# Performance work log

Measured on AMD Instinct MI355X. Metric: run time of the kernel, lower is better.

## Reference

```python
import jax, jax.numpy as jnp
import numpy as np
import math

B, S, H, DK, NB = 2, 128, 4, 128, 4
D = H * DK  # 512


def setup_inputs() -> dict:
    key = jax.random.key(0)
    ks = jax.random.split(key, 24)
    g = lambda i, sh, std=1.0: jax.random.normal(ks[i], sh, jnp.float32) * std
    u = lambda i, sh: jax.random.uniform(ks[i], sh, jnp.float32)
    return {
        "x_m": g(0, (B, S, D)), "x_c": g(1, (B, S, D)),
        "b_m": g(2, (B, S, D)), "b_c": g(3, (B, S, D)),
        "bb_m": g(4, (B, NB, NB, D)), "bb_c": u(5, (B, NB, NB, D)),
        "p_m": g(6, (B, S, D)), "p_c": u(7, (B, S, D)),
        "W_xm": g(8, (3, D, H, DK), 0.02), "W_xc": g(9, (3, D, H, DK), 0.02),
        "W_bm": g(10, (3, D, H, DK), 0.02), "W_bc": g(11, (3, D, H, DK), 0.02),
        "Wq1_w": g(12, (DK, DK), 0.05), "Wq1_b": g(13, (DK,), 0.02),
        "Wq2_w": g(14, (DK, DK), 0.05), "Wq2_b": g(15, (DK,), 0.02),
        "Wk1_w": g(16, (DK, DK), 0.05), "Wk1_b": g(17, (DK,), 0.02),
        "Wk2_w": g(18, (DK, DK), 0.05), "Wk2_b": g(19, (DK,), 0.02),
        "mean_w": g(20, (D, D), 0.02), "mean_b": jnp.zeros((D,), jnp.float32),
        "cov_w": g(21, (D, D), 0.02), "cov_b": jnp.zeros((D,), jnp.float32),
        "ln_w": jnp.ones((D,), jnp.float32), "ln_b": jnp.zeros((D,), jnp.float32),
        "b_seq": jax.random.randint(ks[22], (B, S), 0, NB),
    }


def _elu1(x):
    return jax.nn.elu(x) + 1.0


def _tri_sagp(m1, m2, m3, c1, c2, c3):
    # fuse three diagonal Gaussians by product-of-Gaussians (precision-weighted)
    eps = 1e-24
    p1 = 1.0 / jnp.clip(c1, eps)
    p2 = 1.0 / jnp.clip(c2, eps)
    p3 = 1.0 / jnp.clip(c3, eps)
    c = 1.0 / (p1 + p2 + p3)
    return c * (m1 * p1 + m2 * p2 + m3 * p3), c


def _ln(x, w, b):
    m = jnp.mean(x, -1, keepdims=True)
    v = jnp.mean((x - m) ** 2, -1, keepdims=True)
    return (x - m) / jnp.sqrt(v + 1e-12) * w + b


def _forward(x_m, x_c, b_m, b_c, bb_m, bb_c, p_m, p_c,
             W_xm, W_xc, W_bm, W_bc,
             Wq1_w, Wq1_b, Wq2_w, Wq2_b, Wk1_w, Wk1_b, Wk2_w, Wk2_b,
             mean_w, mean_b, cov_w, cov_b, ln_w, ln_b, b_seq):
    Bb, Ss, Dd = x_m.shape
    Hh, Dk = W_xm.shape[2], W_xm.shape[3]
    proj = lambda x, w: jnp.einsum('bnd,dhk->bhnk', x, w)
    q1 = proj(x_m, W_xm[0]) + proj(b_m, W_bm[0])
    k1 = proj(x_m, W_xm[1]) + proj(b_m, W_bm[1])
    v1 = proj(x_m, W_xm[2]) + proj(b_m, W_bm[2])
    q2 = _elu1(proj(x_c, W_xc[0]) + proj(b_c, W_bc[0]))
    k2 = _elu1(proj(x_c, W_xc[1]) + proj(b_c, W_bc[1]))
    v2 = _elu1(proj(x_c, W_xc[2]) + proj(b_c, W_bc[2]))
    nb = bb_m.shape[1]
    # [B,NB,NB,D] -> [B,H,NB,NB,DK]
    bbm = bb_m.reshape(Bb, nb, nb, Hh, Dk).transpose(0, 3, 1, 2, 4)
    bbc = bb_c.reshape(Bb, nb, nb, Hh, Dk).transpose(0, 3, 1, 2, 4)
    # out[b,h,i,j,:] = bbm[b,h,b_seq[b,j],b_seq[b,i],:]  (matches torch advanced indexing + permute)
    gather = jax.vmap(lambda bb, seq: bb[:, seq[None, :], seq[:, None], :])
    bbm_b = gather(bbm, b_seq)  # [B,H,S,S,DK]
    bbc_b = gather(bbc, b_seq)
    pm = p_m.reshape(Bb, Ss, Hh, Dk).transpose(0, 2, 1, 3)  # [B,H,S,DK]
    pc = p_c.reshape(Bb, Ss, Hh, Dk).transpose(0, 2, 1, 3)
    lin = lambda x, w, b: x @ w.T + b
    fQm, fQc = _tri_sagp(q1[:, :, :, None, :], lin(bbm_b, Wq1_w, Wq1_b),
                         lin(pm, Wq2_w, Wq2_b)[:, :, :, None, :],
                         q2[:, :, :, None, :], bbc_b, pc[:, :, :, None, :])
    fKm, fKc = _tri_sagp(k1[:, :, None, :, :], lin(bbm_b, Wk1_w, Wk1_b),
                         lin(pm, Wk2_w, Wk2_b)[:, :, None, :, :],
                         k2[:, :, None, :, :], bbc_b, pc[:, :, None, :, :])
    eps = 1e-24
    # 2-Wasserstein^2 between diagonal Gaussians (the 1x1 matmul form reduces to this)
    w2 = jnp.sum((fQm - fKm) ** 2, -1) + jnp.sum(
        (jnp.sqrt(jnp.clip(fQc, eps)) - jnp.sqrt(jnp.clip(fKc, eps))) ** 2, -1)
    scores = -w2 / math.sqrt(Dk)  # [B,H,S,S]
    probs = jax.nn.softmax(scores, axis=-1)
    mean_ctx = jnp.einsum('bhij,bhjk->bhik', probs, v1)
    cov_ctx = jnp.einsum('bhij,bhjk->bhik', probs ** 2, v2)
    mean_ctx = mean_ctx.transpose(0, 2, 1, 3).reshape(Bb, Ss, Dd)
    cov_ctx = cov_ctx.transpose(0, 2, 1, 3).reshape(Bb, Ss, Dd)
    mean_h = _ln(mean_ctx @ mean_w.T + mean_b + x_m, ln_w, ln_b)
    cov_h = _ln(cov_ctx @ cov_w.T + cov_b + x_c, ln_w, ln_b)
    return mean_h, cov_h, probs


def reference(x_m, x_c, b_m, b_c, bb_m, bb_c, p_m, p_c,
              W_xm, W_xc, W_bm, W_bc,
              Wq1_w, Wq1_b, Wq2_w, Wq2_b, Wk1_w, Wk1_b, Wk2_w, Wk2_b,
              mean_w, mean_b, cov_w, cov_b, ln_w, ln_b, b_seq):
    return _forward(x_m, x_c, b_m, b_c, bb_m, bb_c, p_m, p_c,
                    W_xm, W_xc, W_bm, W_bc,
                    Wq1_w, Wq1_b, Wq2_w, Wq2_b, Wk1_w, Wk1_b, Wk2_w, Wk2_b,
                    mean_w, mean_b, cov_w, cov_b, ln_w, ln_b, b_seq)
```

## Files before the change

### kernel.cpp

```cpp
#include <hip/hip_runtime.h>
#include <math.h>

#define B_ 2
#define S_ 128
#define H_ 4
#define DK_ 128
#define NB_ 4
#define D_ 512
#define M_ 256

typedef __attribute__((ext_vector_type(8))) short short8;
typedef __attribute__((ext_vector_type(4))) float float4v;
typedef __attribute__((ext_vector_type(4))) unsigned short ushort4v;

__device__ __forceinline__ float elu1(float x) {
    return (x > 0.f) ? (x + 1.f) : __expf(x);
}

__device__ __forceinline__ unsigned short f2bf(float f) {
    unsigned u = __float_as_uint(f);
    unsigned r = (u + 0x7FFFu + ((u >> 16) & 1u)) >> 16;
    return (unsigned short)r;
}


__global__ __launch_bounds__(256) void k_prep(
    const float* __restrict__ x_m, const float* __restrict__ b_m,
    const float* __restrict__ x_c, const float* __restrict__ b_c,
    const float* __restrict__ mean_w, const float* __restrict__ cov_w,
    const float* __restrict__ W_xm, const float* __restrict__ W_xc,
    const float* __restrict__ W_bm, const float* __restrict__ W_bc,
    const float* __restrict__ p_m, const float* __restrict__ bb_m,
    const float* __restrict__ Wq2, const float* __restrict__ Wk2,
    const float* __restrict__ Wq1, const float* __restrict__ Wk1,
    unsigned short* __restrict__ A_m, unsigned short* __restrict__ A_c,
    unsigned short* __restrict__ wm_bf, unsigned short* __restrict__ wc_bf,
    unsigned short* __restrict__ Wt,
    unsigned short* __restrict__ pm_bf, unsigned short* __restrict__ bbm_bf,
    unsigned short* __restrict__ w4_bf)
{
    __shared__ unsigned short tile4[4][32][33];
    const int t = threadIdx.x;
    const int blk = blockIdx.x;
    const int NBK = gridDim.x;

    for (int cid = blk * 256 + t; cid < 315392; cid += NBK * 256) {
        const float* srcp;
        unsigned short* dstp;
        if (cid < 262144) {
            int job = cid >> 16;
            int off = (cid & 65535) * 4;
            if (job <= 1) {
                int m = off >> 10, k = off & 1023;
                if (job == 0) { srcp = (k < 512) ? (x_m + m * 512 + k) : (b_m + m * 512 + k - 512); dstp = A_m + off; }
                else          { srcp = (k < 512) ? (x_c + m * 512 + k) : (b_c + m * 512 + k - 512); dstp = A_c + off; }
            } else if (job == 2) { srcp = mean_w + off; dstp = wm_bf + off; }
            else                 { srcp = cov_w + off;  dstp = wc_bf + off; }
        } else if (cid < 294912) {
            int off = (cid - 262144) * 4;
            srcp = p_m + off; dstp = pm_bf + off;
        } else if (cid < 299008) {
            int off = (cid - 294912) * 4;
            srcp = bb_m + off; dstp = bbm_bf + off;
        } else {
            int off = (cid - 299008) * 4;
            int seg = off >> 14;
            const float* Ws = (seg == 0) ? Wq2 : (seg == 1) ? Wk2 : (seg == 2) ? Wq1 : Wk1;
            srcp = Ws + (off & 16383); dstp = w4_bf + off;
        }
        float4 v = *(const float4*)srcp;
        ushort4v o4;
        o4.x = f2bf(v.x); o4.y = f2bf(v.y); o4.z = f2bf(v.z); o4.w = f2bf(v.w);
        *(ushort4v*)dstp = o4;
    }

    const int tx = t & 31, ty = t >> 5;
#pragma unroll
    for (int it = 0; it < 4; ++it) {
        int tid = blk + it * 768;
        int nt = tid & 15, kt = (tid >> 4) & 15, z = tid >> 8;
        int o = z >> 1, part = z & 1;
        const float* src;
        if (part == 0) src = (o < 3) ? (W_xm + o * 262144) : (W_xc + (o - 3) * 262144);
        else           src = (o < 3) ? (W_bm + o * 262144) : (W_bc + (o - 3) * 262144);
#pragma unroll
        for (int u = 0; u < 4; ++u)
            tile4[it][ty + u * 8][tx] = f2bf(src[(kt * 32 + ty + u * 8) * 512 + nt * 32 + tx]);
    }
    __syncthreads();
#pragma unroll
    for (int it = 0; it < 4; ++it) {
        int tid = blk + it * 768;
        int nt = tid & 15, kt = (tid >> 4) & 15, z = tid >> 8;
        int o = z >> 1, part = z & 1;
        unsigned short* dst = Wt + o * 524288 + part * 512;
#pragma unroll
        for (int u = 0; u < 4; ++u)
            dst[(nt * 32 + ty + u * 8) * 1024 + kt * 32 + tx] = tile4[it][tx][ty + u * 8];
    }
}

__global__ __launch_bounds__(256) void k_mm(
    const unsigned short* __restrict__ A_m, const unsigned short* __restrict__ A_c,
    const unsigned short* __restrict__ Wt,
    const unsigned short* __restrict__ pm_bf, const unsigned short* __restrict__ bbm_bf,
    const unsigned short* __restrict__ w4_bf,
    const float* __restrict__ bq2, const float* __restrict__ bk2,
    const float* __restrict__ bq1, const float* __restrict__ bk1,
    float* __restrict__ qkv, float* __restrict__ pq, float* __restrict__ pk,
    float* __restrict__ bbq, float* __restrict__ bbk)
{
    const int t = threadIdx.x;
    const int wid = blockIdx.x * 4 + (t >> 6);
    const int lane = t & 63;
    const int l15 = lane & 15, quad = lane >> 4;

    if (wid < 3072) {
        const int o = wid >> 9;
        const int rem = wid & 511;
        const int nt = rem & 31, mt = rem >> 5;
        const int m0 = mt * 16, n0 = nt * 16;

        const unsigned short* A = (o < 3) ? A_m : A_c;
        const unsigned short* ap = A + (m0 + l15) * 1024 + quad * 8;
        const unsigned short* bp = Wt + o * 524288 + (n0 + l15) * 1024 + quad * 8;

        float4v acc0 = {0.f, 0.f, 0.f, 0.f};
        float4v acc1 = {0.f, 0.f, 0.f, 0.f};
#pragma unroll
        for (int k0 = 0; k0 < 1024; k0 += 64) {
            short8 a0 = *(const short8*)(ap + k0);
            short8 b0 = *(const short8*)(bp + k0);
            short8 a1 = *(const short8*)(ap + k0 + 32);
            short8 b1 = *(const short8*)(bp + k0 + 32);
            acc0 = __builtin_amdgcn_mfma_f32_16x16x32_bf16(a0, b0, acc0, 0, 0, 0);
            acc1 = __builtin_amdgcn_mfma_f32_16x16x32_bf16(a1, b1, acc1, 0, 0, 0);
        }
        float* dst = qkv + o * 131072;
#pragma unroll
        for (int r = 0; r < 4; ++r) {
            float v = acc0[r] + acc1[r];
            if (o >= 3) v = elu1(v);
            dst[(m0 + quad * 4 + r) * 512 + n0 + l15] = v;
        }
    } else {
        const unsigned short* Abf;
        const unsigned short* Wb;
        const float* bias;
        float* dst;
        int m0, n0, h;
        if (wid < 4096) {
            int lid = wid - 3072;
            int sel = lid >> 9;
            int r = lid & 511;
            h = r >> 7;
            int rem = r & 127;
            m0 = (rem >> 3) * 16; n0 = (rem & 7) * 16;
            Abf = pm_bf;
            Wb = w4_bf + sel * 16384;
            bias = sel ? bk2 : bq2;
            dst = sel ? pk : pq;
        } else {
            int lid = wid - 4096;
            int sel = lid >> 6;
            int r = lid & 63;
            h = r >> 4;
            int rem = r & 15;
            m0 = (rem >> 3) * 16; n0 = (rem & 7) * 16;
            Abf = bbm_bf;
            Wb = w4_bf + 32768 + sel * 16384;
            bias = sel ? bk1 : bq1;
            dst = sel ? bbk : bbq;
        }
        const unsigned short* ap = Abf + (m0 + l15) * 512 + h * 128 + quad * 8;
        const unsigned short* bp = Wb + (n0 + l15) * 128 + quad * 8;

        float4v acc0 = {0.f, 0.f, 0.f, 0.f};
        float4v acc1 = {0.f, 0.f, 0.f, 0.f};
#pragma unroll
        for (int k0 = 0; k0 < 128; k0 += 64) {
            short8 a0 = *(const short8*)(ap + k0);
            short8 b0 = *(const short8*)(bp + k0);
            short8 a1 = *(const short8*)(ap + k0 + 32);
            short8 b1 = *(const short8*)(bp + k0 + 32);
            acc0 = __builtin_amdgcn_mfma_f32_16x16x32_bf16(a0, b0, acc0, 0, 0, 0);
            acc1 = __builtin_amdgcn_mfma_f32_16x16x32_bf16(a1, b1, acc1, 0, 0, 0);
        }
        float bv = bias[n0 + l15];
#pragma unroll
        for (int r = 0; r < 4; ++r)
            dst[(m0 + quad * 4 + r) * 512 + h * 128 + n0 + l15] = acc0[r] + acc1[r] + bv;
    }
}

__global__ __launch_bounds__(128) void k_fuseK(
    const float* __restrict__ qkv, const float* __restrict__ pk,
    const float* __restrict__ bbk, const float* __restrict__ bb_c,
    const float* __restrict__ p_c, const int* __restrict__ b_seq,
    float* __restrict__ fKm, float* __restrict__ fKs)
{
    const int t = threadIdx.x;
    const int j = blockIdx.x, h = blockIdx.y, b = blockIdx.z;
    const int d = h * 128 + t;
    const float eps = 1e-24f;
    const int base = (b * S_ + j) * D_ + d;
    const int sj = b_seq[b * S_ + j];

    float m1 = qkv[M_ * D_ + base];
    float c1 = qkv[4 * M_ * D_ + base];
    float m3 = pk[base];
    float c3 = p_c[base];

    float p1 = 1.f / fmaxf(c1, eps);
    float p3 = 1.f / fmaxf(c3, eps);
    float mp13 = m1 * p1 + m3 * p3;

#pragma unroll
    for (int sv = 0; sv < 4; ++sv) {
        int idx = (b * 16 + sj * 4 + sv) * 512 + d;
        float m2 = bbk[idx];
        float c2 = bb_c[idx];
        float p2 = 1.f / fmaxf(c2, eps);
        float cc = 1.f / (p1 + p2 + p3);
        int o = (((b * H_ + h) * 4 + sv) * S_ + j) * 128 + t;
        fKm[o] = cc * (mp13 + m2 * p2);
        fKs[o] = sqrtf(fmaxf(cc, eps));
    }
}

__global__ __launch_bounds__(128) void k_attn3(
    const float* __restrict__ qkv, const float* __restrict__ pq,
    const float* __restrict__ bbq, const float* __restrict__ bb_c,
    const float* __restrict__ p_c, const int* __restrict__ b_seq,
    const float* __restrict__ fKm, const float* __restrict__ fKs,
    float* __restrict__ probs_out, unsigned short* __restrict__ mctxb,
    unsigned short* __restrict__ cctxb)
{
    const int t = threadIdx.x;
    const int i = blockIdx.x, h = blockIdx.y, b = blockIdx.z;
    const float eps = 1e-24f;

    __shared__ __attribute__((aligned(16))) float qm[4 * 132];
    __shared__ __attribute__((aligned(16))) float qs[4 * 132];
    __shared__ float red[4];
    __shared__ float pr[128], pr2[128];

    const int si = b_seq[b * S_ + i];
    const int sj = b_seq[b * S_ + t];

    {
        const int d = h * 128 + t;
        const int base = (b * S_ + i) * D_ + d;
        float m1 = qkv[base];
        float c1 = qkv[3 * M_ * D_ + base];
        float m3 = pq[base];
        float c3 = p_c[base];
        float p1 = 1.f / fmaxf(c1, eps);
        float p3 = 1.f / fmaxf(c3, eps);
        float mp13 = m1 * p1 + m3 * p3;
#pragma unroll
        for (int sv = 0; sv < 4; ++sv) {
            int idx = (b * 16 + sv * 4 + si) * 512 + d;
            float m2 = bbq[idx];
            float c2 = bb_c[idx];
            float p2 = 1.f / fmaxf(c2, eps);
            float cc = 1.f / (p1 + p2 + p3);
            qm[sv * 132 + t] = cc * (mp13 + m2 * p2);
            qs[sv * 132 + t] = sqrtf(fmaxf(cc, eps));
        }
    }
    __syncthreads();

    const int krow = (((b * H_ + h) * 4 + si) * S_ + t) * 128;
    const float4* kmp = (const float4*)(fKm + krow);
    const float4* ksp = (const float4*)(fKs + krow);

    float w2 = 0.f;
#pragma unroll 4
    for (int k4 = 0; k4 < 32; ++k4) {
        float4 km = kmp[k4];
        float4 ks = ksp[k4];
        float4 m = *(const float4*)&qm[sj * 132 + k4 * 4];
        float4 s = *(const float4*)&qs[sj * 132 + k4 * 4];
        float d0 = m.x - km.x, d1 = m.y - km.y, d2 = m.z - km.z, d3 = m.w - km.w;
        float e0 = s.x - ks.x, e1 = s.y - ks.y, e2 = s.z - ks.z, e3 = s.w - ks.w;
        w2 += d0 * d0 + d1 * d1 + d2 * d2 + d3 * d3
            + e0 * e0 + e1 * e1 + e2 * e2 + e3 * e3;
    }
    float score = -w2 * 0.08838834764831845f;

    float mx = score;
#pragma unroll
    for (int off = 32; off >= 1; off >>= 1) mx = fmaxf(mx, __shfl_xor(mx, off));
    if ((t & 63) == 0) red[t >> 6] = mx;
    __syncthreads();
    mx = fmaxf(red[0], red[1]);
    float e = __expf(score - mx);
    float sm = e;
#pragma unroll
    for (int off = 32; off >= 1; off >>= 1) sm += __shfl_xor(sm, off);
    if ((t & 63) == 0) red[2 + (t >> 6)] = sm;
    __syncthreads();
    float p = e / (red[2] + red[3]);

    probs_out[((b * H_ + h) * S_ + i) * S_ + t] = p;
    pr[t] = p;
    pr2[t] = p * p;
    __syncthreads();

    const float* v1 = qkv + 2 * M_ * D_ + (b * S_) * D_ + h * 128 + t;
    const float* v2 = qkv + 5 * M_ * D_ + (b * S_) * D_ + h * 128 + t;
    float am = 0.f, ac = 0.f;
#pragma unroll 8
    for (int j = 0; j < 128; ++j) {
        am = fmaf(pr[j], v1[j * D_], am);
        ac = fmaf(pr2[j], v2[j * D_], ac);
    }
    mctxb[(b * S_ + i) * D_ + h * 128 + t] = f2bf(am);
    cctxb[(b * S_ + i) * D_ + h * 128 + t] = f2bf(ac);
}

__global__ __launch_bounds__(256) void k_fin_mm(
    const unsigned short* __restrict__ mctxb, const unsigned short* __restrict__ cctxb,
    const unsigned short* __restrict__ wm_bf, const unsigned short* __restrict__ wc_bf,
    float* __restrict__ y_m, float* __restrict__ y_c)
{
    const int t = threadIdx.x;
    const int wid = blockIdx.x * 4 + (t >> 6);
    const int lane = t & 63;
    const int mat = wid >> 9;
    const int rem = wid & 511;
    const int nt = rem & 31, mt = rem >> 5;
    const int m0 = mt * 16, n0 = nt * 16;
    const int l15 = lane & 15, quad = lane >> 4;

    const unsigned short* A = mat ? cctxb : mctxb;
    const unsigned short* Bw = mat ? wc_bf : wm_bf;
    float* y = mat ? y_c : y_m;

    const unsigned short* ap = A + (m0 + l15) * 512 + quad * 8;
    const unsigned short* bp = Bw + (n0 + l15) * 512 + quad * 8;

    float4v acc0 = {0.f, 0.f, 0.f, 0.f};
    float4v acc1 = {0.f, 0.f, 0.f, 0.f};
#pragma unroll
    for (int k0 = 0; k0 < 512; k0 += 64) {
        short8 a0 = *(const short8*)(ap + k0);
        short8 b0 = *(const short8*)(bp + k0);
        short8 a1 = *(const short8*)(ap + k0 + 32);
        short8 b1 = *(const short8*)(bp + k0 + 32);
        acc0 = __builtin_amdgcn_mfma_f32_16x16x32_bf16(a0, b0, acc0, 0, 0, 0);
        acc1 = __builtin_amdgcn_mfma_f32_16x16x32_bf16(a1, b1, acc1, 0, 0, 0);
    }
#pragma unroll
    for (int r = 0; r < 4; ++r)
        y[(m0 + quad * 4 + r) * 512 + n0 + l15] = acc0[r] + acc1[r];
}

__global__ __launch_bounds__(256) void k_ln(
    const float* __restrict__ y_m, const float* __restrict__ y_c,
    const float* __restrict__ mean_b, const float* __restrict__ cov_b,
    const float* __restrict__ x_m, const float* __restrict__ x_c,
    const float* __restrict__ ln_w, const float* __restrict__ ln_b,
    float* __restrict__ out)
{
    const int t = threadIdx.x;
    const int id = blockIdx.x;
    const int mat = id >> 8, row = id & 255;
    const float* yg = mat ? y_c : y_m;
    const float* bias = mat ? cov_b : mean_b;
    const float* res = mat ? x_c : x_m;
    const int base = row * 512;

    __shared__ float red[8];

    float y0 = yg[base + t] + bias[t] + res[base + t];
    float y1 = yg[base + 256 + t] + bias[256 + t] + res[base + 256 + t];
    float s = y0 + y1, ss = y0 * y0 + y1 * y1;
#pragma unroll
    for (int off = 32; off >= 1; off >>= 1) { s += __shfl_xor(s, off); ss += __shfl_xor(ss, off); }
    if ((t & 63) == 0) { red[t >> 6] = s; red[4 + (t >> 6)] = ss; }
    __syncthreads();
    float mu = (red[0] + red[1] + red[2] + red[3]) * (1.f / 512.f);
    float var = (red[4] + red[5] + red[6] + red[7]) * (1.f / 512.f) - mu * mu;
    float rstd = 1.f / sqrtf(var + 1e-12f);
    out[mat * 131072 + base + t] = (y0 - mu) * rstd * ln_w[t] + ln_b[t];
    out[mat * 131072 + base + 256 + t] = (y1 - mu) * rstd * ln_w[256 + t] + ln_b[256 + t];
}

extern "C" void kernel_launch(void* const* d_in, const int* in_sizes, int n_in,
                              void* d_out, int out_size, void* d_ws, size_t ws_size,
                              hipStream_t stream) {
    (void)in_sizes; (void)n_in; (void)out_size; (void)ws_size;
    const float* x_m   = (const float*)d_in[0];
    const float* x_c   = (const float*)d_in[1];
    const float* b_m   = (const float*)d_in[2];
    const float* b_c   = (const float*)d_in[3];
    const float* bb_m  = (const float*)d_in[4];
    const float* bb_c  = (const float*)d_in[5];
    const float* p_m   = (const float*)d_in[6];
    const float* p_c   = (const float*)d_in[7];
    const float* W_xm  = (const float*)d_in[8];
    const float* W_xc  = (const float*)d_in[9];
    const float* W_bm  = (const float*)d_in[10];
    const float* W_bc  = (const float*)d_in[11];
    const float* Wq1_w = (const float*)d_in[12];
    const float* Wq1_b = (const float*)d_in[13];
    const float* Wq2_w = (const float*)d_in[14];
    const float* Wq2_b = (const float*)d_in[15];
    const float* Wk1_w = (const float*)d_in[16];
    const float* Wk1_b = (const float*)d_in[17];
    const float* Wk2_w = (const float*)d_in[18];
    const float* Wk2_b = (const float*)d_in[19];
    const float* mean_w = (const float*)d_in[20];
    const float* mean_b = (const float*)d_in[21];
    const float* cov_w  = (const float*)d_in[22];
    const float* cov_b  = (const float*)d_in[23];
    const float* ln_w   = (const float*)d_in[24];
    const float* ln_b   = (const float*)d_in[25];
    const int*   b_seq  = (const int*)d_in[26];

    float* ws = (float*)d_ws;
    float* qkv = ws;
    float* pq  = ws + 786432;
    float* pk  = ws + 917504;
    float* bbq = ws + 1048576;
    float* bbk = ws + 1064960;
    float* fKm = ws + 1081344;
    float* fKs = ws + 1605632;
    float* y_m = ws + 2129920;
    float* y_c = ws + 2260992;
    unsigned short* A_m    = (unsigned short*)(ws + 2392064);
    unsigned short* A_c    = (unsigned short*)(ws + 2523136);
    unsigned short* Wt     = (unsigned short*)(ws + 2654208);
    unsigned short* wm_bf  = (unsigned short*)(ws + 4227072);
    unsigned short* wc_bf  = (unsigned short*)(ws + 4358144);
    unsigned short* mctxb  = (unsigned short*)(ws + 4489216);
    unsigned short* cctxb  = (unsigned short*)(ws + 4554752);
    unsigned short* pm_bf  = (unsigned short*)(ws + 4620288);
    unsigned short* bbm_bf = (unsigned short*)(ws + 4685824);
    unsigned short* w4_bf  = (unsigned short*)(ws + 4694016);
    float* out = (float*)d_out;

    k_prep<<<dim3(768), 256, 0, stream>>>(
        x_m, b_m, x_c, b_c, mean_w, cov_w, W_xm, W_xc, W_bm, W_bc,
        p_m, bb_m, Wq2_w, Wk2_w, Wq1_w, Wk1_w,
        A_m, A_c, wm_bf, wc_bf, Wt, pm_bf, bbm_bf, w4_bf);
    k_mm<<<dim3(1056), 256, 0, stream>>>(
        A_m, A_c, Wt, pm_bf, bbm_bf, w4_bf,
        Wq2_b, Wk2_b, Wq1_b, Wk1_b,
        qkv, pq, pk, bbq, bbk);
    k_fuseK<<<dim3(128, 4, 2), 128, 0, stream>>>(
        qkv, pk, bbk, bb_c, p_c, b_seq, fKm, fKs);
    k_attn3<<<dim3(128, 4, 2), 128, 0, stream>>>(
        qkv, pq, bbq, bb_c, p_c, b_seq, fKm, fKs, out + 262144, mctxb, cctxb);
    k_fin_mm<<<dim3(256), 256, 0, stream>>>(
        mctxb, cctxb, wm_bf, wc_bf, y_m, y_c);
    k_ln<<<dim3(512), 256, 0, stream>>>(
        y_m, y_c, mean_b, cov_b, x_m, x_c, ln_w, ln_b, out);
}
```

Measured before the change: 176.0 us.

## Widen QKV GEMM wave tiles to 16x32, swizzle blocks for XCD locality

Each wave in the main projection GEMM now computes a 16x32 output tile, reusing the A fragment across two B column tiles, which halves the wave count and the redundant A loads. The first 384 blocks are remapped with a stride permutation so that blocks landing on the same XCD share A/W rows in cache. The attention kernel moves from a 3D grid to a 1D grid with batch and head interleaved in the low bits, also aimed at cache locality across XCDs. The cost is more accumulator registers per wave and fewer waves to hide memory latency.

After: 176.2 us, median of 2. No clear change (+0.1%).

```diff
diff --git a/kernel.cpp b/kernel.cpp
--- a/kernel.cpp
+++ b/kernel.cpp
@@ -111,37 +111,48 @@
     float* __restrict__ bbq, float* __restrict__ bbk)
 {
     const int t = threadIdx.x;
-    const int wid = blockIdx.x * 4 + (t >> 6);
+    const int blk = blockIdx.x;
+    const int sblk = (blk < 384) ? ((blk & 7) * 48 + (blk >> 3)) : blk;
+    const int wid = sblk * 4 + (t >> 6);
     const int lane = t & 63;
     const int l15 = lane & 15, quad = lane >> 4;
 
-    if (wid < 3072) {
-        const int o = wid >> 9;
-        const int rem = wid & 511;
-        const int nt = rem & 31, mt = rem >> 5;
-        const int m0 = mt * 16, n0 = nt * 16;
+    if (wid < 1536) {
+        const int o = wid >> 8;
+        const int rem = wid & 255;
+        const int nt2 = rem & 15, mt = rem >> 4;
+        const int m0 = mt * 16, n0 = nt2 * 32;
 
         const unsigned short* A = (o < 3) ? A_m : A_c;
-        const unsigned short* ap = A + (m0 + l15) * 1024 + quad * 8;
-        const unsigned short* bp = Wt + o * 524288 + (n0 + l15) * 1024 + quad * 8;
-
-        float4v acc0 = {0.f, 0.f, 0.f, 0.f};
-        float4v acc1 = {0.f, 0.f, 0.f, 0.f};
+        const unsigned short* ap  = A + (m0 + l15) * 1024 + quad * 8;
+        const unsigned short* bpa = Wt + o * 524288 + (n0 + l15) * 1024 + quad * 8;
+        const unsigned short* bpb = bpa + 16 * 1024;
+
+        float4v accA0 = {0.f, 0.f, 0.f, 0.f};
+        float4v accA1 = {0.f, 0.f, 0.f, 0.f};
+        float4v accB0 = {0.f, 0.f, 0.f, 0.f};
+        float4v accB1 = {0.f, 0.f, 0.f, 0.f};
 #pragma unroll
         for (int k0 = 0; k0 < 1024; k0 += 64) {
             short8 a0 = *(const short8*)(ap + k0);
-            short8 b0 = *(const short8*)(bp + k0);
             short8 a1 = *(const short8*)(ap + k0 + 32);
-            short8 b1 = *(const short8*)(bp + k0 + 32);
-            acc0 = __builtin_amdgcn_mfma_f32_16x16x32_bf16(a0, b0, acc0, 0, 0, 0);
-            acc1 = __builtin_amdgcn_mfma_f32_16x16x32_bf16(a1, b1, acc1, 0, 0, 0);
+            short8 b0a = *(const short8*)(bpa + k0);
+            short8 b1a = *(const short8*)(bpa + k0 + 32);
+            short8 b0b = *(const short8*)(bpb + k0);
+            short8 b1b = *(const short8*)(bpb + k0 + 32);
+            accA0 = __builtin_amdgcn_mfma_f32_16x16x32_bf16(a0, b0a, accA0, 0, 0, 0);
+            accA1 = __builtin_amdgcn_mfma_f32_16x16x32_bf16(a1, b1a, accA1, 0, 0, 0);
+            accB0 = __builtin_amdgcn_mfma_f32_16x16x32_bf16(a0, b0b, accB0, 0, 0, 0);
+            accB1 = __builtin_amdgcn_mfma_f32_16x16x32_bf16(a1, b1b, accB1, 0, 0, 0);
         }
         float* dst = qkv + o * 131072;
 #pragma unroll
         for (int r = 0; r < 4; ++r) {
-            float v = acc0[r] + acc1[r];
-            if (o >= 3) v = elu1(v);
-            dst[(m0 + quad * 4 + r) * 512 + n0 + l15] = v;
+            float va = accA0[r] + accA1[r];
+            float vb = accB0[r] + accB1[r];
+            if (o >= 3) { va = elu1(va); vb = elu1(vb); }
+            dst[(m0 + quad * 4 + r) * 512 + n0 + l15] = va;
+            dst[(m0 + quad * 4 + r) * 512 + n0 + 16 + l15] = vb;
         }
     } else {
         const unsigned short* Abf;
@@ -149,8 +160,8 @@
         const float* bias;
         float* dst;
         int m0, n0, h;
-        if (wid < 4096) {
-            int lid = wid - 3072;
+        if (wid < 2560) {
+            int lid = wid - 1536;
             int sel = lid >> 9;
             int r = lid & 511;
             h = r >> 7;
@@ -161,7 +172,7 @@
             bias = sel ? bk2 : bq2;
             dst = sel ? pk : pq;
         } else {
-            int lid = wid - 4096;
+            int lid = wid - 2560;
             int sel = lid >> 6;
             int r = lid & 63;
             h = r >> 4;
@@ -237,7 +248,10 @@
     unsigned short* __restrict__ cctxb)
 {
     const int t = threadIdx.x;
-    const int i = blockIdx.x, h = blockIdx.y, b = blockIdx.z;
+    const int blk = blockIdx.x;
+    const int bh = blk & 7;
+    const int i = blk >> 3;
+    const int b = bh >> 2, h = bh & 3;
     const float eps = 1e-24f;
 
     __shared__ __attribute__((aligned(16))) float qm[4 * 132];
@@ -446,13 +460,13 @@
         x_m, b_m, x_c, b_c, mean_w, cov_w, W_xm, W_xc, W_bm, W_bc,
         p_m, bb_m, Wq2_w, Wk2_w, Wq1_w, Wk1_w,
         A_m, A_c, wm_bf, wc_bf, Wt, pm_bf, bbm_bf, w4_bf);
-    k_mm<<<dim3(1056), 256, 0, stream>>>(
+    k_mm<<<dim3(672), 256, 0, stream>>>(
         A_m, A_c, Wt, pm_bf, bbm_bf, w4_bf,
         Wq2_b, Wk2_b, Wq1_b, Wk1_b,
         qkv, pq, pk, bbq, bbk);
     k_fuseK<<<dim3(128, 4, 2), 128, 0, stream>>>(
         qkv, pk, bbk, bb_c, p_c, b_seq, fKm, fKs);
-    k_attn3<<<dim3(128, 4, 2), 128, 0, stream>>>(
+    k_attn3<<<dim3(1024), 128, 0, stream>>>(
         qkv, pq, bbq, bb_c, p_c, b_seq, fKm, fKs, out + 262144, mctxb, cctxb);
     k_fin_mm<<<dim3(256), 256, 0, stream>>>(
         mctxb, cctxb, wm_bf, wc_bf, y_m, y_c);
```
